# Performance work log

Hardware: AMD Instinct MI355X
Metric: run time of the kernel (lower is better)

## Reference

```python
import jax, jax.numpy as jnp
import numpy as np

B, L, D, H = 2, 1024, 1024, 16
HEAD = D // H
BUCKETS = 256
MAX_REL = 512
ATT_SPAN = BUCKETS          # pos_ebd_size = position_buckets when buckets > 0
SCALE_FACTOR = 3            # 1 (content) + 1 (c2p) + 1 (p2c)


def _log_bucket(rel, bucket_size, max_position):
    """make_log_bucket_position: signed log-bucketed relative positions."""
    sign = jnp.sign(rel).astype(jnp.float32)
    mid = bucket_size // 2
    abs_pos = jnp.where((rel < mid) & (rel > -mid), mid - 1, jnp.abs(rel)).astype(jnp.float32)
    log_pos = jnp.ceil(jnp.log(abs_pos / mid) / np.float32(np.log((max_position - 1) / mid)) * (mid - 1)) + mid
    bucket = jnp.where(abs_pos <= mid, rel.astype(jnp.float32), log_pos * sign)
    return bucket.astype(jnp.int32)


def build_relative_position(q_len, k_len):
    rel = jnp.arange(q_len, dtype=jnp.int32)[:, None] - jnp.arange(k_len, dtype=jnp.int32)[None, :]
    return _log_bucket(rel, BUCKETS, MAX_REL)  # [q_len, k_len]


def setup_inputs() -> dict:
    key = jax.random.key(0)
    ks = jax.random.split(key, 6)
    w = 0.02  # typical init scale, keeps softmax well-conditioned
    return {
        "hidden_states": jax.random.normal(ks[0], (B, L, D), jnp.float32),
        "attention_mask": jnp.ones((B, L), jnp.int32),
        "rel_embeddings": jax.random.normal(ks[1], (2 * ATT_SPAN, D), jnp.float32) * w,
        "Wq": jax.random.normal(ks[2], (D, D), jnp.float32) * w,
        "bq": jnp.zeros((D,), jnp.float32),
        "Wk": jax.random.normal(ks[3], (D, D), jnp.float32) * w,
        "bk": jnp.zeros((D,), jnp.float32),
        "Wv": jax.random.normal(ks[4], (D, D), jnp.float32) * w,
        "bv": jnp.zeros((D,), jnp.float32),
    }


def reference(hidden_states, attention_mask, rel_embeddings, Wq, bq, Wk, bk, Wv, bv):
    Bn, Ln, Dn = hidden_states.shape

    def proj(x, W, b):  # Linear with bias, torch convention y = x W^T + b
        return x @ W.T + b

    def to_heads(x):  # [.., L, D] -> [.., H, L, HEAD]
        return x.reshape(*x.shape[:-1], H, HEAD).swapaxes(-3, -2)

    q = to_heads(proj(hidden_states, Wq, bq))  # [B,H,L,d]
    k = to_heads(proj(hidden_states, Wk, bk))
    v = to_heads(proj(hidden_states, Wv, bv))

    scale = jnp.sqrt(jnp.float32(HEAD * SCALE_FACTOR))
    scores = jnp.einsum('bhqd,bhkd->bhqk', q, k) / scale

    # disentangled relative-position bias (share_att_key=True -> reuse Wq/Wk)
    rel = build_relative_position(Ln, Ln)                     # [L,L] log-bucketed
    pos_k = proj(rel_embeddings, Wk, bk).reshape(2 * ATT_SPAN, H, HEAD)
    pos_q = proj(rel_embeddings, Wq, bq).reshape(2 * ATT_SPAN, H, HEAD)

    # c2p: Q . posK, gathered at (rel + span)
    c2p_att = jnp.einsum('bhqd,phd->bhqp', q, pos_k)          # [B,H,L,2S]
    c2p_idx = jnp.clip(rel + ATT_SPAN, 0, 2 * ATT_SPAN - 1)   # [L,L]
    c2p = jnp.take_along_axis(c2p_att, jnp.broadcast_to(c2p_idx[None, None], (Bn, H, Ln, Ln)), axis=-1)

    # p2c: K . posQ gathered at (-rel + span), then transposed to [q,k]
    p2c_att = jnp.einsum('bhkd,phd->bhkp', k, pos_q)          # [B,H,L,2S]
    p2c_idx = jnp.clip(-rel + ATT_SPAN, 0, 2 * ATT_SPAN - 1)
    p2c = jnp.take_along_axis(p2c_att, jnp.broadcast_to(p2c_idx[None, None], (Bn, H, Ln, Ln)), axis=-1)
    p2c = jnp.swapaxes(p2c, -1, -2)

    scores = scores + (c2p + p2c) / scale

    bias = jnp.where(attention_mask[:, None, None, :] > 0, 0.0, -1e9).astype(scores.dtype)
    probs = jax.nn.softmax(scores + bias, axis=-1)
    ctx = jnp.einsum('bhqk,bhkd->bhqd', probs, v)
    return ctx.swapaxes(1, 2).reshape(Bn, Ln, Dn)
```

## Files before the change

### kernel.cpp

```cpp
#include <hip/hip_runtime.h>


typedef short s8v __attribute__((ext_vector_type(8)));
typedef short s4v __attribute__((ext_vector_type(4)));
typedef float f32x4 __attribute__((ext_vector_type(4)));
typedef float f4v __attribute__((ext_vector_type(4)));

#define QK_SCALE 0.26864243f

__device__ __forceinline__ unsigned short f2bf(float f) {
  unsigned u = __builtin_bit_cast(unsigned, f);
  u += 0x7fffu + ((u >> 16) & 1u);
  return (unsigned short)(u >> 16);
}
__device__ __forceinline__ float bf2f(unsigned short h) {
  unsigned u = ((unsigned)h) << 16;
  return __builtin_bit_cast(float, u);
}

__device__ __forceinline__ void gload_lds16(const void* g, void* l) {
  __builtin_amdgcn_global_load_lds(
      (const __attribute__((address_space(1))) void*)g,
      (__attribute__((address_space(3))) void*)l, 16, 0, 0);
}

__global__ __launch_bounds__(256) void prep_kernel(
    const float* __restrict__ hidden, const float* __restrict__ rel,
    const float* __restrict__ Wq, const float* __restrict__ Wk,
    const float* __restrict__ Wv, const int* __restrict__ mask,
    short* __restrict__ Abf, short* __restrict__ Wbf,
    float* __restrict__ mbias, short* __restrict__ Tt) {
  int idx = blockIdx.x * 256 + threadIdx.x;
  const int NCONV = 1441792;
  if (idx < NCONV) {
    const float* src; short* dst; int off;
    if (idx < 524288) { src = hidden; dst = Abf; off = idx; }
    else if (idx < 655360) { src = rel; dst = Abf + 2048 * 1024; off = idx - 524288; }
    else {
      int j = idx - 655360;
      int w = j / 262144; off = j - w * 262144;
      src = (w == 0) ? Wq : (w == 1) ? Wk : Wv;
      dst = Wbf + w * 1048576;
    }
    f4v v = ((const f4v*)src)[off];
    s4v o;
    o[0] = (short)f2bf(v[0]); o[1] = (short)f2bf(v[1]);
    o[2] = (short)f2bf(v[2]); o[3] = (short)f2bf(v[3]);
    ((s4v*)dst)[off] = o;
  } else {
    int j = idx - NCONV;
    if (j < 2047) {
      int r = j - 1023;
      float fr = (float)r;
      float sign = (r > 0) ? 1.f : ((r < 0) ? -1.f : 0.f);
      float abs_pos = (r < 128 && r > -128) ? 127.f : fabsf(fr);
      const float logc = 1.3843393245589053f;
      float log_pos = ceilf(logf(abs_pos * (1.f / 128.f)) / logc * 127.f) + 128.f;
      float bucket = (abs_pos <= 128.f) ? fr : log_pos * sign;
      int bi = (int)bucket + 256;
      bi = bi < 0 ? 0 : (bi > 511 ? 511 : bi);
      Tt[j] = (short)bi;
    } else if (j < 4095) {
      int m = j - 2047;
      mbias[m] = (mask[m] > 0) ? 0.f : -1e9f;
    }
  }
}

__global__ __launch_bounds__(256) void gemm_qkv(
    const short* __restrict__ Abf, const short* __restrict__ Wbf,
    const float* __restrict__ bq, const float* __restrict__ bk,
    const float* __restrict__ bv,
    short* __restrict__ Qc, short* __restrict__ Kc, short* __restrict__ Vc) {
  __shared__ short As[128 * 64];
  __shared__ short Bs[128 * 64];
  int tid = threadIdx.x;
  int wid = tid >> 6, lane = tid & 63;
  int lr = lane & 15, lg = lane >> 4;
  int wr = wid >> 1, wc = wid & 1;
  int z = blockIdx.z;
  int brow = blockIdx.y * 128;
  if (z == 2 && brow >= 2048) return;
  const short* W = Wbf + z * 1048576;
  const float* bias = (z == 0) ? bq : (z == 1) ? bk : bv;
  short* C = (z == 0) ? Qc : (z == 1) ? Kc : Vc;
  float scale = (z == 2) ? 1.f : QK_SCALE;
  int bcol = blockIdx.x * 128;

  f32x4 acc[4][4];
  for (int i = 0; i < 4; i++)
    for (int j = 0; j < 4; j++) acc[i][j] = (f32x4){0.f, 0.f, 0.f, 0.f};

  for (int k0 = 0; k0 < 1024; k0 += 64) {
    for (int i = 0; i < 4; i++) {
      int n = i * 256 + wid * 64 + lane;
      const short* gA = Abf + (size_t)(brow + (n >> 3)) * 1024 + k0 + (n & 7) * 8;
      gload_lds16(gA, &As[(i * 256 + wid * 64) * 8]);
      const short* gB = W + (size_t)(bcol + (n >> 3)) * 1024 + k0 + (n & 7) * 8;
      gload_lds16(gB, &Bs[(i * 256 + wid * 64) * 8]);
    }
    __syncthreads();
    for (int ks = 0; ks < 2; ks++) {
      s8v af[4], bfv[4];
      for (int mi = 0; mi < 4; mi++)
        af[mi] = *(const s8v*)&As[(wr * 64 + mi * 16 + lr) * 64 + ks * 32 + lg * 8];
      for (int ni = 0; ni < 4; ni++)
        bfv[ni] = *(const s8v*)&Bs[(wc * 64 + ni * 16 + lr) * 64 + ks * 32 + lg * 8];
      for (int mi = 0; mi < 4; mi++)
        for (int ni = 0; ni < 4; ni++)
          acc[mi][ni] = __builtin_amdgcn_mfma_f32_16x16x32_bf16(
              af[mi], bfv[ni], acc[mi][ni], 0, 0, 0);
    }
    __syncthreads();
  }
  for (int mi = 0; mi < 4; mi++)
    for (int ni = 0; ni < 4; ni++) {
      int col = bcol + wc * 64 + ni * 16 + lr;
      float bb = bias[col];
      for (int r = 0; r < 4; r++) {
        int row = brow + wr * 64 + mi * 16 + lg * 4 + r;
        float v = (acc[mi][ni][r] + bb) * scale;
        C[(size_t)row * 1024 + col] = (short)f2bf(v);
      }
    }
}

__global__ __launch_bounds__(256) void pos_gemm(
    const short* __restrict__ Qc, const short* __restrict__ Kc,
    const float* __restrict__ mbias,
    short* __restrict__ c2p, short* __restrict__ p2c) {
  __shared__ short As[128 * 64];
  __shared__ short Bs[128 * 64];
  int tid = threadIdx.x;
  int wid = tid >> 6, lane = tid & 63;
  int lr = lane & 15, lg = lane >> 4;
  int wr = wid >> 1, wc = wid & 1;
  int zz = blockIdx.z;
  int which = zz >> 5;
  int bh = zz & 31;
  int b = bh >> 4, h = bh & 15;
  const short* Arows = (which == 0) ? Qc : Kc;
  const short* Brows = (which == 0) ? Kc : Qc;
  short* Out = (which == 0) ? c2p : p2c;
  int mrow = blockIdx.y * 128;
  int ncol = blockIdx.x * 128;

  for (int i = 0; i < 4; i++) {
    int n = i * 256 + wid * 64 + lane;
    const short* gA = Arows + (size_t)(b * 1024 + mrow + (n >> 3)) * 1024 + h * 64 + (n & 7) * 8;
    gload_lds16(gA, &As[(i * 256 + wid * 64) * 8]);
    const short* gB = Brows + (size_t)(2048 + ncol + (n >> 3)) * 1024 + h * 64 + (n & 7) * 8;
    gload_lds16(gB, &Bs[(i * 256 + wid * 64) * 8]);
  }
  __syncthreads();

  f32x4 acc[4][4];
  for (int i = 0; i < 4; i++)
    for (int j = 0; j < 4; j++) acc[i][j] = (f32x4){0.f, 0.f, 0.f, 0.f};
  for (int ks = 0; ks < 2; ks++) {
    s8v af[4], bfv[4];
    for (int mi = 0; mi < 4; mi++)
      af[mi] = *(const s8v*)&As[(wr * 64 + mi * 16 + lr) * 64 + ks * 32 + lg * 8];
    for (int ni = 0; ni < 4; ni++)
      bfv[ni] = *(const s8v*)&Bs[(wc * 64 + ni * 16 + lr) * 64 + ks * 32 + lg * 8];
    for (int mi = 0; mi < 4; mi++)
      for (int ni = 0; ni < 4; ni++)
        acc[mi][ni] = __builtin_amdgcn_mfma_f32_16x16x32_bf16(
            af[mi], bfv[ni], acc[mi][ni], 0, 0, 0);
  }
  size_t base = (size_t)(b * 16 + h) * 1024;
  for (int mi = 0; mi < 4; mi++)
    for (int ni = 0; ni < 4; ni++)
      for (int r = 0; r < 4; r++) {
        int m = mrow + wr * 64 + mi * 16 + lg * 4 + r;
        int nn = ncol + wc * 64 + ni * 16 + lr;
        float v = acc[mi][ni][r];
        if (which == 1) v += mbias[b * 1024 + m];
        Out[(base + m) * 512 + nn] = (short)f2bf(v);
      }
}

__global__ __launch_bounds__(256) void transpose_v(
    const short* __restrict__ Vc, short* __restrict__ Vt) {
  __shared__ short TL[64 * 72];
  int tid = threadIdx.x;
  int lt = blockIdx.x, h = blockIdx.y, b = blockIdx.z;
  for (int i = 0; i < 2; i++) {
    int n = i * 256 + tid;
    int l = n >> 3, c = n & 7;
    s8v v = *(const s8v*)&Vc[(size_t)(b * 1024 + lt * 64 + l) * 1024 + h * 64 + c * 8];
    *(s8v*)&TL[l * 72 + c * 8] = v;
  }
  __syncthreads();
  for (int i = 0; i < 2; i++) {
    int m = i * 256 + tid;
    int d = m >> 3, c = m & 7;
    s8v o;
    for (int jj = 0; jj < 8; jj++) o[jj] = TL[(c * 8 + jj) * 72 + d];
    *(s8v*)&Vt[((size_t)(b * 16 + h) * 64 + d) * 1024 + lt * 64 + c * 8] = o;
  }
}

__global__ __launch_bounds__(256) void bias_build(
    const short* __restrict__ c2p, const short* __restrict__ p2c,
    const short* __restrict__ Tt, short* __restrict__ bias) {
  __shared__ short Wc[64 * 66];
  __shared__ short Wp[64 * 66];
  __shared__ short Tl[128];
  int tid = threadIdx.x;
  int wid = tid >> 6, lane = tid & 63;
  int lr = lane & 15, lg = lane >> 4;
  int qt = blockIdx.x, kt = blockIdx.y, bh = blockIdx.z;
  int q0 = qt * 64, k0 = kt * 64;
  int relbase = q0 - k0;
  size_t bh1024 = (size_t)bh * 1024;

  if (tid < 127) Tl[tid] = Tt[relbase + 960 + tid];
  __syncthreads();

#pragma unroll
  for (int ii = 0; ii < 16; ii++) {
    int row = wid * 16 + ii;
    int w0 = Tl[row];
    int col = w0 + lane; col = col > 511 ? 511 : col;
    Wc[row * 66 + lane] = c2p[(bh1024 + q0 + row) * 512 + col];
    int w0p_ = Tl[63 - row];
    int colp = w0p_ + lane; colp = colp > 511 ? 511 : colp;
    Wp[row * 66 + lane] = p2c[(bh1024 + k0 + row) * 512 + colp];
  }
  __syncthreads();

  int w0c[4], w0p[4];
#pragma unroll
  for (int r = 0; r < 4; r++) w0c[r] = Tl[wid * 16 + lg * 4 + r];
#pragma unroll
  for (int n = 0; n < 4; n++) w0p[n] = Tl[63 - (n * 16 + lr)];

  s8v o0, o1;
#pragma unroll
  for (int n = 0; n < 4; n++)
#pragma unroll
    for (int r = 0; r < 4; r++) {
      int qq = wid * 16 + lg * 4 + r;
      int kk = n * 16 + lr;
      int p = Tl[qq - kk + 63];
      float v = bf2f((unsigned short)Wc[qq * 66 + p - w0c[r]]) +
                bf2f((unsigned short)Wp[kk * 66 + p - w0p[n]]);
      short s = (short)f2bf(v);
      if (n < 2) o0[(n & 1) * 4 + r] = s; else o1[(n & 1) * 4 + r] = s;
    }
  size_t tile = ((size_t)bh * 16 + qt) * 16 + kt;
  size_t base = (tile * 4 + wid) * 1024 + lane * 8;
  *(s8v*)&bias[base] = o0;
  *(s8v*)&bias[base + 512] = o1;
}

template <int NSPLIT>
__global__ __launch_bounds__(256) void attn_frag(
    const short* __restrict__ Qc, const short* __restrict__ Kc,
    const short* __restrict__ Vt, const short* __restrict__ bias,
    float* __restrict__ Opart, float* __restrict__ dpart,
    float* __restrict__ out) {
  const int KSEG = 1024 / NSPLIT;
  const int NT = KSEG / 64;
  __shared__ short Kl[2][64 * 64];
  __shared__ short Vl[2][64 * 64];
  __shared__ short Pl[4][16 * 72];
  int tid = threadIdx.x;
  int wid = tid >> 6, lane = tid & 63;
  int lr = lane & 15, lg = lane >> 4;
  int qt = blockIdx.x, h = blockIdx.y, z = blockIdx.z;
  int b = (NSPLIT == 1) ? z : (z >> 2);
  int ks = (NSPLIT == 1) ? 0 : (z & 3);
  int k0seg = ks * KSEG;
  int q0 = qt * 64, qbase = q0 + wid * 16;

  s8v aq[2];
  for (int s_ = 0; s_ < 2; s_++)
    aq[s_] = *(const s8v*)&Qc[(size_t)(b * 1024 + qbase + lr) * 1024 + h * 64 + s_ * 32 + lg * 8];

  f32x4 oacc[4];
  for (int n = 0; n < 4; n++) oacc[n] = (f32x4){0.f, 0.f, 0.f, 0.f};
  float dsum[4] = {0.f, 0.f, 0.f, 0.f};

  auto stage = [&](int t, int buf) {
#pragma unroll
    for (int i = 0; i < 2; i++) {
      int n = i * 256 + tid;
      int row = n >> 3, cswz = n & 7, cb = cswz ^ (row & 7);
      gload_lds16(&Kc[(size_t)(b * 1024 + k0seg + t * 64 + row) * 1024 + h * 64 + cb * 8],
                  &Kl[buf][(i * 256 + wid * 64) * 8]);
      gload_lds16(&Vt[((size_t)(b * 16 + h) * 64 + row) * 1024 + k0seg + t * 64 + cb * 8],
                  &Vl[buf][(i * 256 + wid * 64) * 8]);
    }
  };
  auto fload = [&](int t, s8v& f0, s8v& f1) {
    size_t tile = (((size_t)(b * 16 + h) * 16 + qt) * 16 + (k0seg >> 6) + t);
    size_t base = (tile * 4 + wid) * 1024 + lane * 8;
    f0 = *(const s8v*)&bias[base];
    f1 = *(const s8v*)&bias[base + 512];
  };

  s8v fb0, fb1, fn0, fn1;
  stage(0, 0);
  fload(0, fb0, fb1);
  __syncthreads();

#pragma unroll
  for (int t = 0; t < NT; ++t) {
    const int cur = t & 1, nxt = cur ^ 1;

    if (t + 1 < NT) {
      stage(t + 1, nxt);
      fload(t + 1, fn0, fn1);
    }

    f32x4 sacc[4];
#pragma unroll
    for (int n = 0; n < 4; n++) sacc[n] = (f32x4){0.f, 0.f, 0.f, 0.f};
#pragma unroll
    for (int s_ = 0; s_ < 2; s_++)
#pragma unroll
      for (int n = 0; n < 4; n++) {
        int row = n * 16 + lr, cb = s_ * 4 + lg, cbs = cb ^ (row & 7);
        s8v bk_ = *(const s8v*)&Kl[cur][row * 64 + cbs * 8];
        sacc[n] = __builtin_amdgcn_mfma_f32_16x16x32_bf16(aq[s_], bk_, sacc[n], 0, 0, 0);
      }

#pragma unroll
    for (int n = 0; n < 4; n++)
#pragma unroll
      for (int r = 0; r < 4; r++) {
        unsigned short bv_ = (unsigned short)((n < 2 ? fb0 : fb1)[(n & 1) * 4 + r]);
        float p = __expf(sacc[n][r] + bf2f(bv_));
        dsum[r] += p;
        Pl[wid][(lg * 4 + r) * 72 + n * 16 + lr] = (short)f2bf(p);
      }
    asm volatile("s_waitcnt lgkmcnt(0)" ::: "memory");

#pragma unroll
    for (int s_ = 0; s_ < 2; s_++) {
      s8v ap = *(const s8v*)&Pl[wid][lr * 72 + s_ * 32 + lg * 8];
#pragma unroll
      for (int n = 0; n < 4; n++) {
        int row = n * 16 + lr, cb = s_ * 4 + lg, cbs = cb ^ (row & 7);
        s8v bv_ = *(const s8v*)&Vl[cur][row * 64 + cbs * 8];
        oacc[n] = __builtin_amdgcn_mfma_f32_16x16x32_bf16(ap, bv_, oacc[n], 0, 0, 0);
      }
    }

    __syncthreads();

    if (t + 1 < NT) { fb0 = fn0; fb1 = fn1; }
  }

  for (int m = 1; m < 16; m <<= 1)
    for (int r = 0; r < 4; r++) dsum[r] += __shfl_xor(dsum[r], m, 64);

  if (NSPLIT == 1) {
    for (int n = 0; n < 4; n++)
      for (int r = 0; r < 4; r++) {
        int q = qbase + lg * 4 + r;
        int d = n * 16 + lr;
        out[(size_t)(b * 1024 + q) * 1024 + h * 64 + d] = oacc[n][r] / dsum[r];
      }
  } else {
    size_t po = ((size_t)(z * 16 + h)) * 65536;
    for (int n = 0; n < 4; n++)
      for (int r = 0; r < 4; r++) {
        int q = qbase + lg * 4 + r;
        Opart[po + (size_t)q * 64 + n * 16 + lr] = oacc[n][r];
      }
    if (lr == 0)
      for (int r = 0; r < 4; r++)
        dpart[(z * 16 + h) * 1024 + qbase + lg * 4 + r] = dsum[r];
  }
}

template <int NSPLIT>
__global__ __launch_bounds__(256) void attn_gather(
    const short* __restrict__ Qc, const short* __restrict__ Kc,
    const short* __restrict__ Vt, const short* __restrict__ c2p,
    const short* __restrict__ p2c, const short* __restrict__ Tt,
    float* __restrict__ Opart, float* __restrict__ dpart,
    float* __restrict__ out) {
  const int KSEG = 1024 / NSPLIT;
  const int NT = KSEG / 64;
  const int TLN = 64 + KSEG - 1;
  __shared__ short Kl[2][64 * 64];
  __shared__ short Vl[2][64 * 64];
  __shared__ short Pl[4][16 * 72];
  __shared__ short Tl[TLN + 1];
  int tid = threadIdx.x;
  int wid = tid >> 6, lane = tid & 63;
  int lr = lane & 15, lg = lane >> 4;
  int qt = blockIdx.x, h = blockIdx.y, z = blockIdx.z;
  int b = (NSPLIT == 1) ? z : (z >> 2);
  int ks = (NSPLIT == 1) ? 0 : (z & 3);
  int k0seg = ks * KSEG;
  int q0 = qt * 64, qbase = q0 + wid * 16;
  size_t bh1024 = (size_t)(b * 16 + h) * 1024;

  for (int i = tid; i < TLN; i += 256) Tl[i] = Tt[(q0 - k0seg - (KSEG - 1) + 1023) + i];

  s8v aq[2];
  for (int s_ = 0; s_ < 2; s_++)
    aq[s_] = *(const s8v*)&Qc[(size_t)(b * 1024 + qbase + lr) * 1024 + h * 64 + s_ * 32 + lg * 8];

  f32x4 oacc[4];
  for (int n = 0; n < 4; n++) oacc[n] = (f32x4){0.f, 0.f, 0.f, 0.f};
  float dsum[4] = {0.f, 0.f, 0.f, 0.f};
  __syncthreads();

  auto stage = [&](int t, int buf) {
#pragma unroll
    for (int i = 0; i < 2; i++) {
      int n = i * 256 + tid;
      int row = n >> 3, cswz = n & 7, cb = cswz ^ (row & 7);
      gload_lds16(&Kc[(size_t)(b * 1024 + k0seg + t * 64 + row) * 1024 + h * 64 + cb * 8],
                  &Kl[buf][(i * 256 + wid * 64) * 8]);
      gload_lds16(&Vt[((size_t)(b * 16 + h) * 64 + row) * 1024 + k0seg + t * 64 + cb * 8],
                  &Vl[buf][(i * 256 + wid * 64) * 8]);
    }
  };
  auto gather = [&](int t, unsigned short* cg, unsigned short* pg) {
#pragma unroll
    for (int n = 0; n < 4; n++) {
      int k = k0seg + t * 64 + n * 16 + lr;
      size_t prow = (bh1024 + k) * 512;
      int jb = wid * 16 - t * 64 - lr + (KSEG - 1) - n * 16 + lg * 4;
#pragma unroll
      for (int r = 0; r < 4; r++) {
        int q = qbase + lg * 4 + r;
        int idx = Tl[jb + r];
        cg[n * 4 + r] = (unsigned short)c2p[(bh1024 + q) * 512 + idx];
        pg[n * 4 + r] = (unsigned short)p2c[prow + idx];
      }
    }
  };

  unsigned short c2g[16], p2g[16], c2n[16], p2n[16];
  stage(0, 0);
  gather(0, c2g, p2g);
  __syncthreads();

#pragma unroll
  for (int t = 0; t < NT; ++t) {
    const int cur = t & 1, nxt = cur ^ 1;
    if (t + 1 < NT) { stage(t + 1, nxt); gather(t + 1, c2n, p2n); }

    f32x4 sacc[4];
#pragma unroll
    for (int n = 0; n < 4; n++) sacc[n] = (f32x4){0.f, 0.f, 0.f, 0.f};
#pragma unroll
    for (int s_ = 0; s_ < 2; s_++)
#pragma unroll
      for (int n = 0; n < 4; n++) {
        int row = n * 16 + lr, cb = s_ * 4 + lg, cbs = cb ^ (row & 7);
        s8v bk_ = *(const s8v*)&Kl[cur][row * 64 + cbs * 8];
        sacc[n] = __builtin_amdgcn_mfma_f32_16x16x32_bf16(aq[s_], bk_, sacc[n], 0, 0, 0);
      }
#pragma unroll
    for (int n = 0; n < 4; n++)
#pragma unroll
      for (int r = 0; r < 4; r++) {
        float bias = bf2f(c2g[n * 4 + r]) + bf2f(p2g[n * 4 + r]);
        float p = __expf(sacc[n][r] + bias);
        dsum[r] += p;
        Pl[wid][(lg * 4 + r) * 72 + n * 16 + lr] = (short)f2bf(p);
      }
    asm volatile("s_waitcnt lgkmcnt(0)" ::: "memory");
#pragma unroll
    for (int s_ = 0; s_ < 2; s_++) {
      s8v ap = *(const s8v*)&Pl[wid][lr * 72 + s_ * 32 + lg * 8];
#pragma unroll
      for (int n = 0; n < 4; n++) {
        int row = n * 16 + lr, cb = s_ * 4 + lg, cbs = cb ^ (row & 7);
        s8v bv_ = *(const s8v*)&Vl[cur][row * 64 + cbs * 8];
        oacc[n] = __builtin_amdgcn_mfma_f32_16x16x32_bf16(ap, bv_, oacc[n], 0, 0, 0);
      }
    }
    __syncthreads();
    if (t + 1 < NT) {
#pragma unroll
      for (int i = 0; i < 16; i++) { c2g[i] = c2n[i]; p2g[i] = p2n[i]; }
    }
  }

  for (int m = 1; m < 16; m <<= 1)
    for (int r = 0; r < 4; r++) dsum[r] += __shfl_xor(dsum[r], m, 64);

  if (NSPLIT == 1) {
    for (int n = 0; n < 4; n++)
      for (int r = 0; r < 4; r++) {
        int q = qbase + lg * 4 + r;
        int d = n * 16 + lr;
        out[(size_t)(b * 1024 + q) * 1024 + h * 64 + d] = oacc[n][r] / dsum[r];
      }
  } else {
    size_t po = ((size_t)(z * 16 + h)) * 65536;
    for (int n = 0; n < 4; n++)
      for (int r = 0; r < 4; r++) {
        int q = qbase + lg * 4 + r;
        Opart[po + (size_t)q * 64 + n * 16 + lr] = oacc[n][r];
      }
    if (lr == 0)
      for (int r = 0; r < 4; r++)
        dpart[(z * 16 + h) * 1024 + qbase + lg * 4 + r] = dsum[r];
  }
}

__global__ __launch_bounds__(256) void combine_kernel(
    const float* __restrict__ Opart, const float* __restrict__ dpart,
    float* __restrict__ out) {
  int idx = blockIdx.x * 256 + threadIdx.x;
  int pos = idx * 4;
  int b = pos >> 20;
  int q = (pos >> 10) & 1023;
  int hd = pos & 1023;
  int h = hd >> 6, d = hd & 63;
  f4v s = (f4v){0.f, 0.f, 0.f, 0.f};
  float dn = 0.f;
  for (int ks = 0; ks < 4; ks++) {
    int zh = (b * 4 + ks) * 16 + h;
    s += *(const f4v*)&Opart[(size_t)zh * 65536 + q * 64 + d];
    dn += dpart[zh * 1024 + q];
  }
  f4v r = s / dn;
  *(f4v*)&out[pos] = r;
}

extern "C" void kernel_launch(void* const* d_in, const int* in_sizes, int n_in,
                              void* d_out, int out_size, void* d_ws, size_t ws_size,
                              hipStream_t stream) {
  (void)in_sizes; (void)n_in; (void)out_size;
  const float* hidden = (const float*)d_in[0];
  const int* mask = (const int*)d_in[1];
  const float* rel = (const float*)d_in[2];
  const float* Wq = (const float*)d_in[3];
  const float* bq = (const float*)d_in[4];
  const float* Wk = (const float*)d_in[5];
  const float* bk = (const float*)d_in[6];
  const float* Wv = (const float*)d_in[7];
  const float* bv = (const float*)d_in[8];
  float* out = (float*)d_out;

  char* w = (char*)d_ws;
  short* Abf = (short*)w; w += 2560 * 1024 * 2;
  short* Wbf = (short*)w; w += 3 * 1024 * 1024 * 2;
  short* Qc  = (short*)w; w += 2560 * 1024 * 2;
  short* Kc  = (short*)w; w += 2560 * 1024 * 2;
  short* Vc  = (short*)w; w += 2560 * 1024 * 2;
  short* Vt  = (short*)w; w += 2 * 16 * 64 * 1024 * 2;
  short* c2p = (short*)w; w += (size_t)2 * 16 * 1024 * 512 * 2;
  short* p2c = (short*)w; w += (size_t)2 * 16 * 1024 * 512 * 2;
  short* Tt  = (short*)w; w += 4096;
  float* mbias = (float*)w; w += 8192;
  short* bias_frag = (short*)w;
  size_t need_frag = (size_t)(w - (char*)d_ws) + (size_t)8192 * 4096 * 2;
  float* Opart_old = (float*)w;
  size_t need_old = (size_t)(w - (char*)d_ws) + (size_t)8 * 16 * 1024 * 64 * 4 + 8 * 16 * 1024 * 4;

  prep_kernel<<<5648, 256, 0, stream>>>(hidden, rel, Wq, Wk, Wv, mask, Abf, Wbf, mbias, Tt);
  gemm_qkv<<<dim3(8, 20, 3), 256, 0, stream>>>(Abf, Wbf, bq, bk, bv, Qc, Kc, Vc);
  pos_gemm<<<dim3(4, 8, 64), 256, 0, stream>>>(Qc, Kc, mbias, c2p, p2c);
  transpose_v<<<dim3(16, 16, 2), 256, 0, stream>>>(Vc, Vt);

  if (ws_size >= need_frag) {
    float* Opart = (float*)c2p;
    float* dpart = (float*)p2c;
    bias_build<<<dim3(16, 16, 32), 256, 0, stream>>>(c2p, p2c, Tt, bias_frag);
    attn_frag<4><<<dim3(16, 16, 8), 256, 0, stream>>>(Qc, Kc, Vt, bias_frag,
                                                      Opart, dpart, out);
    combine_kernel<<<2048, 256, 0, stream>>>(Opart, dpart, out);
  } else if (ws_size >= need_old) {
    float* Opart = Opart_old;
    float* dpart = (float*)((char*)Opart_old + (size_t)8 * 16 * 1024 * 64 * 4);
    attn_gather<4><<<dim3(16, 16, 8), 256, 0, stream>>>(Qc, Kc, Vt, c2p, p2c, Tt,
                                                        Opart, dpart, out);
    combine_kernel<<<2048, 256, 0, stream>>>(Opart, dpart, out);
  } else {
    attn_gather<1><<<dim3(16, 16, 2), 256, 0, stream>>>(Qc, Kc, Vt, c2p, p2c, Tt,
                                                        (float*)Opart_old, (float*)Opart_old, out);
  }
}
```

Measured before the change: 149.5 us.

## Swizzle QKV GEMM LDS tiles and halve attention key-split count

The QKV projection GEMM now applies an XOR swizzle to the 16-byte column chunks it stages into LDS and reads back with the same swizzle, to cut LDS bank conflicts on fragment loads. Separately, the fragment-bias attention path drops from four key splits to two, and the combine kernel is templated on the split count. Fewer splits mean less partial-output traffic and combine work, but also half as many attention blocks, so the GPU may be less fully occupied.

```diff
diff --git a/kernel.cpp b/kernel.cpp
--- a/kernel.cpp
+++ b/kernel.cpp
@@ -94,18 +94,23 @@
   for (int k0 = 0; k0 < 1024; k0 += 64) {
     for (int i = 0; i < 4; i++) {
       int n = i * 256 + wid * 64 + lane;
-      const short* gA = Abf + (size_t)(brow + (n >> 3)) * 1024 + k0 + (n & 7) * 8;
+      int row = n >> 3, cswz = n & 7, cb = cswz ^ (row & 7);
+      const short* gA = Abf + (size_t)(brow + row) * 1024 + k0 + cb * 8;
       gload_lds16(gA, &As[(i * 256 + wid * 64) * 8]);
-      const short* gB = W + (size_t)(bcol + (n >> 3)) * 1024 + k0 + (n & 7) * 8;
+      const short* gB = W + (size_t)(bcol + row) * 1024 + k0 + cb * 8;
       gload_lds16(gB, &Bs[(i * 256 + wid * 64) * 8]);
     }
     __syncthreads();
     for (int ks = 0; ks < 2; ks++) {
       s8v af[4], bfv[4];
-      for (int mi = 0; mi < 4; mi++)
-        af[mi] = *(const s8v*)&As[(wr * 64 + mi * 16 + lr) * 64 + ks * 32 + lg * 8];
-      for (int ni = 0; ni < 4; ni++)
-        bfv[ni] = *(const s8v*)&Bs[(wc * 64 + ni * 16 + lr) * 64 + ks * 32 + lg * 8];
+      for (int mi = 0; mi < 4; mi++) {
+        int row = wr * 64 + mi * 16 + lr, cb = ks * 4 + lg;
+        af[mi] = *(const s8v*)&As[row * 64 + (cb ^ (row & 7)) * 8];
+      }
+      for (int ni = 0; ni < 4; ni++) {
+        int row = wc * 64 + ni * 16 + lr, cb = ks * 4 + lg;
+        bfv[ni] = *(const s8v*)&Bs[row * 64 + (cb ^ (row & 7)) * 8];
+      }
       for (int mi = 0; mi < 4; mi++)
         for (int ni = 0; ni < 4; ni++)
           acc[mi][ni] = __builtin_amdgcn_mfma_f32_16x16x32_bf16(
@@ -270,8 +275,8 @@
   int wid = tid >> 6, lane = tid & 63;
   int lr = lane & 15, lg = lane >> 4;
   int qt = blockIdx.x, h = blockIdx.y, z = blockIdx.z;
-  int b = (NSPLIT == 1) ? z : (z >> 2);
-  int ks = (NSPLIT == 1) ? 0 : (z & 3);
+  int b = (NSPLIT == 1) ? z : (z / NSPLIT);
+  int ks = (NSPLIT == 1) ? 0 : (z % NSPLIT);
   int k0seg = ks * KSEG;
   int q0 = qt * 64, qbase = q0 + wid * 16;
 
@@ -395,8 +400,8 @@
   int wid = tid >> 6, lane = tid & 63;
   int lr = lane & 15, lg = lane >> 4;
   int qt = blockIdx.x, h = blockIdx.y, z = blockIdx.z;
-  int b = (NSPLIT == 1) ? z : (z >> 2);
-  int ks = (NSPLIT == 1) ? 0 : (z & 3);
+  int b = (NSPLIT == 1) ? z : (z / NSPLIT);
+  int ks = (NSPLIT == 1) ? 0 : (z % NSPLIT);
   int k0seg = ks * KSEG;
   int q0 = qt * 64, qbase = q0 + wid * 16;
   size_t bh1024 = (size_t)(b * 16 + h) * 1024;
@@ -510,6 +515,7 @@
   }
 }
 
+template <int NSPLIT>
 __global__ __launch_bounds__(256) void combine_kernel(
     const float* __restrict__ Opart, const float* __restrict__ dpart,
     float* __restrict__ out) {
@@ -521,8 +527,8 @@
   int h = hd >> 6, d = hd & 63;
   f4v s = (f4v){0.f, 0.f, 0.f, 0.f};
   float dn = 0.f;
-  for (int ks = 0; ks < 4; ks++) {
-    int zh = (b * 4 + ks) * 16 + h;
+  for (int ks = 0; ks < NSPLIT; ks++) {
+    int zh = (b * NSPLIT + ks) * 16 + h;
     s += *(const f4v*)&Opart[(size_t)zh * 65536 + q * 64 + d];
     dn += dpart[zh * 1024 + q];
   }
@@ -570,15 +576,15 @@
     float* Opart = (float*)c2p;
     float* dpart = (float*)p2c;
     bias_build<<<dim3(16, 16, 32), 256, 0, stream>>>(c2p, p2c, Tt, bias_frag);
-    attn_frag<4><<<dim3(16, 16, 8), 256, 0, stream>>>(Qc, Kc, Vt, bias_frag,
+    attn_frag<2><<<dim3(16, 16, 4), 256, 0, stream>>>(Qc, Kc, Vt, bias_frag,
                                                       Opart, dpart, out);
-    combine_kernel<<<2048, 256, 0, stream>>>(Opart, dpart, out);
+    combine_kernel<2><<<2048, 256, 0, stream>>>(Opart, dpart, out);
   } else if (ws_size >= need_old) {
     float* Opart = Opart_old;
     float* dpart = (float*)((char*)Opart_old + (size_t)8 * 16 * 1024 * 64 * 4);
     attn_gather<4><<<dim3(16, 16, 8), 256, 0, stream>>>(Qc, Kc, Vt, c2p, p2c, Tt,
                                                         Opart, dpart, out);
-    combine_kernel<<<2048, 256, 0, stream>>>(Opart, dpart, out);
+    combine_kernel<4><<<2048, 256, 0, stream>>>(Opart, dpart, out);
   } else {
     attn_gather<1><<<dim3(16, 16, 2), 256, 0, stream>>>(Qc, Kc, Vt, c2p, p2c, Tt,
                                                         (float*)Opart_old, (float*)Opart_old, out);
```

Result: faster. 140.4 us (-6.1%).
